# Optimization experiments

Hardware: AMD Instinct MI355X
Metric: run time of the kernel (lower is better)

## Reference

```python
import jax, jax.numpy as jnp
import numpy as np

DEPTH = 4  # truncation depth of the tensor algebra


def _tprod(a, b):
    # tensor (outer) product of level-i and level-j terms, flattened row-major
    # a: (B, C^i), b: (B, C^j) -> (B, C^(i+j))
    return (a[:, :, None] * b[:, None, :]).reshape(a.shape[0], -1)


def _exp_levels(dx):
    # exp(dx) in the truncated tensor algebra: level k = dx^{\otimes k} / k!
    levels = [dx]
    for k in range(2, DEPTH + 1):
        levels.append(_tprod(levels[-1], dx) / k)
    return tuple(levels)


def _chen(a, b):
    # Chen's identity: (a \otimes b)_k = a_k + b_k + sum_{i=1}^{k-1} a_i \otimes b_{k-i}
    out = []
    for k in range(1, DEPTH + 1):
        t = a[k - 1] + b[k - 1]
        for i in range(1, k):
            t = t + _tprod(a[i - 1], b[k - 1 - i])
        out.append(t)
    return tuple(out)


def _log_levels(s):
    # log(1 + x) = sum_{n>=1} (-1)^{n+1}/n x^{\otimes n}, x = S - 1 (levels 1..DEPTH)
    res = list(s)
    power = [t for t in s]  # x^{\otimes 1}; entries may become None (structurally zero)
    for n in range(2, DEPTH + 1):
        new = [None] * DEPTH
        for k in range(n, DEPTH + 1):
            acc = None
            for i in range(n - 1, k):
                if power[i - 1] is None:
                    continue
                term = _tprod(power[i - 1], s[k - i - 1])
                acc = term if acc is None else acc + term
            new[k - 1] = acc
        power = new
        coef = ((-1.0) ** (n + 1)) / n
        for k in range(n, DEPTH + 1):
            if power[k - 1] is not None:
                res[k - 1] = res[k - 1] + coef * power[k - 1]
    return tuple(res)


def _logsignature(path):
    # path: (B, L, C); no basepoint, stream=False, inverse=False, mode='expand'
    dxs = jnp.moveaxis(path[:, 1:] - path[:, :-1], 1, 0)  # (L-1, B, C)
    init = _exp_levels(dxs[0])

    def step(carry, dx):
        return _chen(carry, _exp_levels(dx)), None

    sig, _ = jax.lax.scan(step, init, dxs[1:])
    logsig = _log_levels(sig)
    return jnp.concatenate(logsig, axis=-1)  # (B, C + C^2 + ... + C^DEPTH)


def setup_inputs() -> dict:
    key = jax.random.key(0)
    # scale so high tensor-algebra levels stay well-conditioned in fp32
    path = 0.1 * jax.random.normal(key, (64, 256, 16), dtype=jnp.float32)
    return {"path": path}


def reference(path):
    return _logsignature(path)
```

## Files before the change

### kernel.cpp

```cpp
#include <hip/hip_runtime.h>


#define NC 16
#define NL 256
#define NB 64
#define NSTEP 255
#define OUTB 69904
#define SIG123 4368
#define OFF_L2 16
#define OFF_L3 272
#define OFF_L4 4368

#define DX1_OFF 0
#define DXT_OFF 261120
#define SIG_OFF (261120 + 262144)

__global__ __launch_bounds__(256) void k_dx(const float* __restrict__ path,
                                            float* __restrict__ dx1,
                                            float* __restrict__ dxt) {
    const int j = blockIdx.x;
    const int tid = threadIdx.x;
    __shared__ float L[NL * NC];

    const float* pj = path + (size_t)j * NL * NC;
#pragma unroll
    for (int k = 0; k < 4; ++k) {
        const int f = tid + k * 256;
        *(float4*)&L[f * 4] = *(const float4*)&pj[f * 4];
    }
    __syncthreads();

    float* d1 = dx1 + (size_t)j * NSTEP * NC;
    for (int f = tid; f < NSTEP * NC; f += 256) d1[f] = L[f + NC] - L[f];

    float* dt = dxt + (size_t)j * NC * 256;
#pragma unroll
    for (int k = 0; k < NC; ++k) {
        const int t = tid;
        if (t < NSTEP) dt[k * 256 + t] = L[(t + 1) * NC + k] - L[t * NC + k];
    }
}

__global__ __launch_bounds__(256, 4) void k_scan(const float* __restrict__ dx1,
                                                 const float* __restrict__ dxt,
                                                 float* __restrict__ out,
                                                 float* __restrict__ sig123) {
    const int bid = blockIdx.x;
    const int j = bid >> 4;
    const int a = bid & 15;
    const int tid = threadIdx.x;
    const int b = tid >> 4;
    const int c = tid & 15;

    float s4[16];
#pragma unroll
    for (int d = 0; d < 16; ++d) s4[d] = 0.f;
    float s3 = 0.f, s2ab = 0.f, s1a = 0.f;

    const float* row0 = dx1 + (size_t)j * NSTEP * NC;
    const float* ra = dxt + ((size_t)j * NC + a) * 256;
    const float* rb = dxt + ((size_t)j * NC + b) * 256;
    const float* rc = dxt + ((size_t)j * NC + c) * 256;

    int t = 0;
    for (int it = 0; it < 63; ++it, t += 4) {
        const float4 vb = *(const float4*)(rb + t);
        const float4 vc = *(const float4*)(rc + t);
        const float4 va = *(const float4*)(ra + t);
#pragma unroll
        for (int u = 0; u < 4; ++u) {
            const float* r = row0 + (t + u) * NC;
            const float4 q0 = *(const float4*)(r);
            const float4 q1 = *(const float4*)(r + 4);
            const float4 q2 = *(const float4*)(r + 8);
            const float4 q3 = *(const float4*)(r + 12);
            const float dxa = (u == 0) ? va.x : (u == 1) ? va.y : (u == 2) ? va.z : va.w;
            const float dxb = (u == 0) ? vb.x : (u == 1) ? vb.y : (u == 2) ? vb.z : vb.w;
            const float dxc = (u == 0) ? vc.x : (u == 1) ? vc.y : (u == 2) ? vc.z : vc.w;

            const float pre4 = fmaf(dxb, fmaf(1.f / 6.f, s1a, (1.f / 24.f) * dxa), 0.5f * s2ab);
            const float T = fmaf(dxc, pre4, s3);
            const float dv[16] = {q0.x, q0.y, q0.z, q0.w, q1.x, q1.y, q1.z, q1.w,
                                  q2.x, q2.y, q2.z, q2.w, q3.x, q3.y, q3.z, q3.w};
#pragma unroll
            for (int d = 0; d < 16; ++d) s4[d] = fmaf(dv[d], T, s4[d]);

            const float U = fmaf(dxb, fmaf(0.5f, s1a, (1.f / 6.f) * dxa), s2ab);
            s3 = fmaf(dxc, U, s3);
            s2ab = fmaf(dxb, fmaf(0.5f, dxa, s1a), s2ab);
            s1a += dxa;
        }
    }
    for (; t < NSTEP; ++t) {
        const float* r = row0 + t * NC;
        const float4 q0 = *(const float4*)(r);
        const float4 q1 = *(const float4*)(r + 4);
        const float4 q2 = *(const float4*)(r + 8);
        const float4 q3 = *(const float4*)(r + 12);
        const float dxa = ra[t];
        const float dxb = rb[t];
        const float dxc = rc[t];
        const float pre4 = fmaf(dxb, fmaf(1.f / 6.f, s1a, (1.f / 24.f) * dxa), 0.5f * s2ab);
        const float T = fmaf(dxc, pre4, s3);
        const float dv[16] = {q0.x, q0.y, q0.z, q0.w, q1.x, q1.y, q1.z, q1.w,
                              q2.x, q2.y, q2.z, q2.w, q3.x, q3.y, q3.z, q3.w};
#pragma unroll
        for (int d = 0; d < 16; ++d) s4[d] = fmaf(dv[d], T, s4[d]);
        const float U = fmaf(dxb, fmaf(0.5f, s1a, (1.f / 6.f) * dxa), s2ab);
        s3 = fmaf(dxc, U, s3);
        s2ab = fmaf(dxb, fmaf(0.5f, dxa, s1a), s2ab);
        s1a += dxa;
    }

    __shared__ float ls[4096];
#pragma unroll
    for (int d = 0; d < 16; d += 4)
        *(float4*)&ls[tid * 16 + d] = make_float4(s4[d], s4[d + 1], s4[d + 2], s4[d + 3]);
    __syncthreads();

    float* o4 = out + (size_t)j * OUTB + OFF_L4 + a * 4096;
#pragma unroll
    for (int k = 0; k < 4; ++k) {
        const int f = tid + k * 256;
        *(float4*)(o4 + f * 4) = *(const float4*)&ls[f * 4];
    }

    float* sg = sig123 + (size_t)j * SIG123;
    sg[OFF_L3 + (a * 16 + b) * 16 + c] = s3;
    if (c == 0) sg[OFF_L2 + a * 16 + b] = s2ab;
    if (tid == 0) sg[a] = s1a;
}

__global__ __launch_bounds__(256) void k_log(const float* __restrict__ sig123,
                                             float* __restrict__ out) {
    const int bid = blockIdx.x;
    const int j = bid >> 4;
    const int a = bid & 15;
    const int tid = threadIdx.x;

    const float* sg = sig123 + (size_t)j * SIG123;
    const float* s1 = sg;
    const float* s2 = sg + OFF_L2;
    const float* s3 = sg + OFF_L3;

    const float s1a = s1[a];
    float* outj = out + (size_t)j * OUTB;
    float* o4 = outj + OFF_L4 + a * 4096;
    const float A = -0.5f * s1a;

#pragma unroll
    for (int k = 0; k < 4; ++k) {
        const int f = tid + k * 256;
        const int m0 = f * 4;
        const int b = m0 >> 8;
        const int c = (m0 >> 4) & 15;
        const float s1b = s1[b], s1c = s1[c];
        const float s2ab = s2[a * 16 + b];
        const float s2bc = s2[b * 16 + c];
        const float s3abc = s3[m0 >> 4];
        const float s3abc_real = s3[(a * 16 + b) * 16 + c];
        (void)s3abc;

        const float Bv = fmaf((1.f / 3.f) * s1a, s1b, -0.5f * s2ab);
        const float Cv = -0.5f * s3abc_real + (1.f / 3.f) * fmaf(s1a, s2bc, s2ab * s1c)
                         - 0.25f * s1a * s1b * s1c;

        const float4 v4 = *(const float4*)(o4 + m0);
        const float4 v3 = *(const float4*)(s3 + m0);
        const float4 v2 = *(const float4*)(s2 + (m0 & 255));
        const float4 v1 = *(const float4*)(s1 + (m0 & 15));
        float4 rr;
        rr.x = fmaf(A, v3.x, v4.x) + fmaf(Bv, v2.x, Cv * v1.x);
        rr.y = fmaf(A, v3.y, v4.y) + fmaf(Bv, v2.y, Cv * v1.y);
        rr.z = fmaf(A, v3.z, v4.z) + fmaf(Bv, v2.z, Cv * v1.z);
        rr.w = fmaf(A, v3.w, v4.w) + fmaf(Bv, v2.w, Cv * v1.w);
        *(float4*)(o4 + m0) = rr;
    }

    {
        const int b = tid >> 4, c = tid & 15;
        const float s1b = s1[b], s1c = s1[c];
        const float s2ab = s2[a * 16 + b];
        const float s2bc = s2[b * 16 + c];
        const float s3abc = s3[(a * 16 + b) * 16 + c];
        const float r3 = s3abc - 0.5f * fmaf(s1a, s2bc, s2ab * s1c)
                         + (1.f / 3.f) * s1a * s1b * s1c;
        outj[OFF_L3 + a * 256 + tid] = r3;
    }
    if (tid < 16) outj[OFF_L2 + a * 16 + tid] = fmaf(-0.5f * s1a, s1[tid], s2[a * 16 + tid]);
    if (tid == 0) outj[a] = s1a;
}

extern "C" void kernel_launch(void* const* d_in, const int* in_sizes, int n_in,
                              void* d_out, int out_size, void* d_ws, size_t ws_size,
                              hipStream_t stream) {
    const float* path = (const float*)d_in[0];
    float* out = (float*)d_out;
    float* ws = (float*)d_ws;
    float* dx1 = ws + DX1_OFF;
    float* dxt = ws + DXT_OFF;
    float* sig123 = ws + SIG_OFF;

    k_dx<<<NB, 256, 0, stream>>>(path, dx1, dxt);
    k_scan<<<NB * 16, 256, 0, stream>>>(dx1, dxt, out, sig123);
    k_log<<<NB * 16, 256, 0, stream>>>(sig123, out);
}
```

Before: 124.9 us.

## Split signature scan over time halves and merge with Chen's identity

```diff
diff --git a/kernel.cpp b/kernel.cpp
--- a/kernel.cpp
+++ b/kernel.cpp
@@ -13,7 +13,10 @@
 
 #define DX1_OFF 0
 #define DXT_OFF 261120
-#define SIG_OFF (261120 + 262144)
+#define SIGA_OFF (261120 + 262144)
+#define SIGB_OFF (SIGA_OFF + NB * SIG123)
+#define B4_OFF (SIGB_OFF + NB * SIG123)
+#define WS_NEED_F ((size_t)B4_OFF + (size_t)NB * 16 * 4096)
 
 __global__ __launch_bounds__(256) void k_dx(const float* __restrict__ path,
                                             float* __restrict__ dx1,
@@ -41,17 +44,25 @@
     }
 }
 
-__global__ __launch_bounds__(256, 4) void k_scan(const float* __restrict__ dx1,
+__global__ __launch_bounds__(256, 8) void k_scan(const float* __restrict__ dx1,
                                                  const float* __restrict__ dxt,
                                                  float* __restrict__ out,
-                                                 float* __restrict__ sig123) {
-    const int bid = blockIdx.x;
+                                                 float* __restrict__ b4,
+                                                 float* __restrict__ sigA,
+                                                 float* __restrict__ sigB,
+                                                 const int split) {
+    int bid = blockIdx.x;
+    int h = 0;
+    if (split) { h = bid & 1; bid >>= 1; }
     const int j = bid >> 4;
     const int a = bid & 15;
     const int tid = threadIdx.x;
     const int b = tid >> 4;
     const int c = tid & 15;
 
+    const int t0 = h ? 128 : 0;
+    const int t1 = (split && !h) ? 128 : NSTEP;
+
     float s4[16];
 #pragma unroll
     for (int d = 0; d < 16; ++d) s4[d] = 0.f;
@@ -62,8 +73,9 @@
     const float* rb = dxt + ((size_t)j * NC + b) * 256;
     const float* rc = dxt + ((size_t)j * NC + c) * 256;
 
-    int t = 0;
-    for (int it = 0; it < 63; ++it, t += 4) {
+    int t = t0;
+    const int nv = (t1 - t0) >> 2;
+    for (int it = 0; it < nv; ++it, t += 4) {
         const float4 vb = *(const float4*)(rb + t);
         const float4 vc = *(const float4*)(rc + t);
         const float4 va = *(const float4*)(ra + t);
@@ -91,7 +103,7 @@
             s1a += dxa;
         }
     }
-    for (; t < NSTEP; ++t) {
+    for (; t < t1; ++t) {
         const float* r = row0 + t * NC;
         const float4 q0 = *(const float4*)(r);
         const float4 q1 = *(const float4*)(r + 4);
@@ -118,76 +130,116 @@
         *(float4*)&ls[tid * 16 + d] = make_float4(s4[d], s4[d + 1], s4[d + 2], s4[d + 3]);
     __syncthreads();
 
-    float* o4 = out + (size_t)j * OUTB + OFF_L4 + a * 4096;
+    float* o4 = h ? (b4 + (((size_t)j * 16 + a) << 12))
+                  : (out + (size_t)j * OUTB + OFF_L4 + a * 4096);
 #pragma unroll
     for (int k = 0; k < 4; ++k) {
         const int f = tid + k * 256;
         *(float4*)(o4 + f * 4) = *(const float4*)&ls[f * 4];
     }
 
-    float* sg = sig123 + (size_t)j * SIG123;
+    float* sg = (h ? sigB : sigA) + (size_t)j * SIG123;
     sg[OFF_L3 + (a * 16 + b) * 16 + c] = s3;
     if (c == 0) sg[OFF_L2 + a * 16 + b] = s2ab;
     if (tid == 0) sg[a] = s1a;
 }
 
-__global__ __launch_bounds__(256) void k_log(const float* __restrict__ sig123,
-                                             float* __restrict__ out) {
+__global__ __launch_bounds__(256) void k_log(const float* __restrict__ sigA,
+                                             const float* __restrict__ sigB,
+                                             const float* __restrict__ b4,
+                                             float* __restrict__ out,
+                                             const float mscale) {
     const int bid = blockIdx.x;
     const int j = bid >> 4;
     const int a = bid & 15;
     const int tid = threadIdx.x;
-
-    const float* sg = sig123 + (size_t)j * SIG123;
-    const float* s1 = sg;
-    const float* s2 = sg + OFF_L2;
-    const float* s3 = sg + OFF_L3;
-
-    const float s1a = s1[a];
+    const int q = tid >> 4;
+    const int r = tid & 15;
+
+    const float* A = sigA + (size_t)j * SIG123;
+    const float* Bp = sigB + (size_t)j * SIG123;
+
+    __shared__ float S1m[16], B1s[16], A2s[16];
+    __shared__ float S2m[256], B2s[256], A3s[256];
+    __shared__ float S3m[4096], B3s[4096];
+
+    const float b1r = mscale * Bp[r];
+    const float b2t = mscale * Bp[OFF_L2 + tid];
+
+    if (tid < 16) {
+        const float bb = mscale * Bp[tid];
+        B1s[tid] = bb;
+        S1m[tid] = A[tid] + bb;
+        A2s[tid] = A[OFF_L2 + a * 16 + tid];
+    }
+    B2s[tid] = b2t;
+    S2m[tid] = A[OFF_L2 + tid] + b2t + A[q] * b1r;
+    A3s[tid] = A[OFF_L3 + a * 256 + tid];
+#pragma unroll
+    for (int k = 0; k < 16; ++k) {
+        const int m = k * 256 + tid;
+        const float b3 = mscale * Bp[OFF_L3 + m];
+        B3s[m] = b3;
+        S3m[m] = A[OFF_L3 + m] + b3 + A[k] * b2t + A[OFF_L2 + k * 16 + q] * b1r;
+    }
+    __syncthreads();
+
+    const float s1a = S1m[a];
+    const float A1a = A[a];
+    const bool mg = (mscale != 0.f);
     float* outj = out + (size_t)j * OUTB;
     float* o4 = outj + OFF_L4 + a * 4096;
-    const float A = -0.5f * s1a;
+    const float* B4 = b4 + (((size_t)j * 16 + a) << 12);
+    const float Ac = -0.5f * s1a;
 
 #pragma unroll
     for (int k = 0; k < 4; ++k) {
         const int f = tid + k * 256;
         const int m0 = f * 4;
-        const int b = m0 >> 8;
-        const int c = (m0 >> 4) & 15;
-        const float s1b = s1[b], s1c = s1[c];
-        const float s2ab = s2[a * 16 + b];
-        const float s2bc = s2[b * 16 + c];
-        const float s3abc = s3[m0 >> 4];
-        const float s3abc_real = s3[(a * 16 + b) * 16 + c];
-        (void)s3abc;
+        const int bb = m0 >> 8;
+        const int cc = (m0 >> 4) & 15;
+        const float s1b = S1m[bb], s1c = S1m[cc];
+        const float s2ab = S2m[a * 16 + bb];
+        const float s2bc = S2m[bb * 16 + cc];
+        const float s3abc = S3m[a * 256 + (m0 >> 4)];
+        const float a3x = A3s[m0 >> 4];
+        const float a2x = A2s[bb];
+
+        const float4 a4 = *(const float4*)(o4 + m0);
+        float4 b4v = make_float4(0.f, 0.f, 0.f, 0.f);
+        if (mg) b4v = *(const float4*)(B4 + m0);
+        const float4 b3v = *(const float4*)(&B3s[m0]);
+        const float4 b2v = *(const float4*)(&B2s[m0 & 255]);
+        const float4 b1v = *(const float4*)(&B1s[m0 & 15]);
+        const float4 v3 = *(const float4*)(&S3m[m0]);
+        const float4 v2 = *(const float4*)(&S2m[m0 & 255]);
+        const float4 v1 = *(const float4*)(&S1m[m0 & 15]);
 
         const float Bv = fmaf((1.f / 3.f) * s1a, s1b, -0.5f * s2ab);
-        const float Cv = -0.5f * s3abc_real + (1.f / 3.f) * fmaf(s1a, s2bc, s2ab * s1c)
+        const float Cv = -0.5f * s3abc + (1.f / 3.f) * fmaf(s1a, s2bc, s2ab * s1c)
                          - 0.25f * s1a * s1b * s1c;
-
-        const float4 v4 = *(const float4*)(o4 + m0);
-        const float4 v3 = *(const float4*)(s3 + m0);
-        const float4 v2 = *(const float4*)(s2 + (m0 & 255));
-        const float4 v1 = *(const float4*)(s1 + (m0 & 15));
         float4 rr;
-        rr.x = fmaf(A, v3.x, v4.x) + fmaf(Bv, v2.x, Cv * v1.x);
-        rr.y = fmaf(A, v3.y, v4.y) + fmaf(Bv, v2.y, Cv * v1.y);
-        rr.z = fmaf(A, v3.z, v4.z) + fmaf(Bv, v2.z, Cv * v1.z);
-        rr.w = fmaf(A, v3.w, v4.w) + fmaf(Bv, v2.w, Cv * v1.w);
+        rr.x = a4.x + b4v.x + fmaf(A1a, b3v.x, fmaf(a2x, b2v.x, a3x * b1v.x));
+        rr.y = a4.y + b4v.y + fmaf(A1a, b3v.y, fmaf(a2x, b2v.y, a3x * b1v.y));
+        rr.z = a4.z + b4v.z + fmaf(A1a, b3v.z, fmaf(a2x, b2v.z, a3x * b1v.z));
+        rr.w = a4.w + b4v.w + fmaf(A1a, b3v.w, fmaf(a2x, b2v.w, a3x * b1v.w));
+        rr.x = fmaf(Ac, v3.x, rr.x) + fmaf(Bv, v2.x, Cv * v1.x);
+        rr.y = fmaf(Ac, v3.y, rr.y) + fmaf(Bv, v2.y, Cv * v1.y);
+        rr.z = fmaf(Ac, v3.z, rr.z) + fmaf(Bv, v2.z, Cv * v1.z);
+        rr.w = fmaf(Ac, v3.w, rr.w) + fmaf(Bv, v2.w, Cv * v1.w);
         *(float4*)(o4 + m0) = rr;
     }
 
     {
-        const int b = tid >> 4, c = tid & 15;
-        const float s1b = s1[b], s1c = s1[c];
-        const float s2ab = s2[a * 16 + b];
-        const float s2bc = s2[b * 16 + c];
-        const float s3abc = s3[(a * 16 + b) * 16 + c];
+        const float s1b = S1m[q], s1c = S1m[r];
+        const float s2ab = S2m[a * 16 + q];
+        const float s2bc = S2m[q * 16 + r];
+        const float s3abc = S3m[a * 256 + tid];
         const float r3 = s3abc - 0.5f * fmaf(s1a, s2bc, s2ab * s1c)
                          + (1.f / 3.f) * s1a * s1b * s1c;
         outj[OFF_L3 + a * 256 + tid] = r3;
     }
-    if (tid < 16) outj[OFF_L2 + a * 16 + tid] = fmaf(-0.5f * s1a, s1[tid], s2[a * 16 + tid]);
+    if (tid < 16) outj[OFF_L2 + a * 16 + tid] = fmaf(-0.5f * s1a, S1m[tid], S2m[a * 16 + tid]);
     if (tid == 0) outj[a] = s1a;
 }
 
@@ -199,9 +251,13 @@
     float* ws = (float*)d_ws;
     float* dx1 = ws + DX1_OFF;
     float* dxt = ws + DXT_OFF;
-    float* sig123 = ws + SIG_OFF;
+    float* sigA = ws + SIGA_OFF;
+
+    const int split = (ws_size >= WS_NEED_F * sizeof(float)) ? 1 : 0;
+    float* sigB = split ? (ws + SIGB_OFF) : sigA;
+    float* b4 = split ? (ws + B4_OFF) : out;
 
     k_dx<<<NB, 256, 0, stream>>>(path, dx1, dxt);
-    k_scan<<<NB * 16, 256, 0, stream>>>(dx1, dxt, out, sig123);
-    k_log<<<NB * 16, 256, 0, stream>>>(sig123, out);
-}
+    k_scan<<<split ? NB * 32 : NB * 16, 256, 0, stream>>>(dx1, dxt, out, b4, sigA, sigB, split);
+    k_log<<<NB * 16, 256, 0, stream>>>(sigA, sigB, b4, out, split ? 1.f : 0.f);
+}
```

After: 135.7 us. 8.7% more time.

## Split signature scan into four time chunks combined via Chen's identity

Applied to the files above, without the earlier changes.

```diff
diff --git a/kernel.cpp b/kernel.cpp
--- a/kernel.cpp
+++ b/kernel.cpp
@@ -4,7 +4,6 @@
 #define NC 16
 #define NL 256
 #define NB 64
-#define NSTEP 255
 #define OUTB 69904
 #define SIG123 4368
 #define OFF_L2 16
@@ -12,8 +11,10 @@
 #define OFF_L4 4368
 
 #define DX1_OFF 0
-#define DXT_OFF 261120
-#define SIG_OFF (261120 + 262144)
+#define DXT_OFF 262144
+#define SIG_OFF 524288
+
+typedef float v2f __attribute__((ext_vector_type(2)));
 
 __global__ __launch_bounds__(256) void k_dx(const float* __restrict__ path,
                                             float* __restrict__ dx1,
@@ -30,43 +31,50 @@
     }
     __syncthreads();
 
-    float* d1 = dx1 + (size_t)j * NSTEP * NC;
-    for (int f = tid; f < NSTEP * NC; f += 256) d1[f] = L[f + NC] - L[f];
+    float* d1 = dx1 + (size_t)j * NL * NC;
+#pragma unroll
+    for (int k = 0; k < 16; ++k) {
+        const int f = tid + k * 256;
+        d1[f] = (f < (NL - 1) * NC) ? (L[f + NC] - L[f]) : 0.f;
+    }
 
     float* dt = dxt + (size_t)j * NC * 256;
 #pragma unroll
     for (int k = 0; k < NC; ++k) {
         const int t = tid;
-        if (t < NSTEP) dt[k * 256 + t] = L[(t + 1) * NC + k] - L[t * NC + k];
-    }
-}
-
-__global__ __launch_bounds__(256, 4) void k_scan(const float* __restrict__ dx1,
+        dt[k * 256 + t] = (t < NL - 1) ? (L[(t + 1) * NC + k] - L[t * NC + k]) : 0.f;
+    }
+}
+
+__global__ __launch_bounds__(512, 8) void k_scan(const float* __restrict__ dx1,
                                                  const float* __restrict__ dxt,
                                                  float* __restrict__ out,
-                                                 float* __restrict__ sig123) {
+                                                 float* __restrict__ sig) {
     const int bid = blockIdx.x;
     const int j = bid >> 4;
     const int a = bid & 15;
     const int tid = threadIdx.x;
-    const int b = tid >> 4;
-    const int c = tid & 15;
-
-    float s4[16];
-#pragma unroll
-    for (int d = 0; d < 16; ++d) s4[d] = 0.f;
-    float s3 = 0.f, s2ab = 0.f, s1a = 0.f;
-
-    const float* row0 = dx1 + (size_t)j * NSTEP * NC;
+    const int qc = tid >> 7;
+    const int b = (tid >> 3) & 15;
+    const int c0 = tid & 7;
+
+    const float* row0 = dx1 + (size_t)j * NL * NC;
     const float* ra = dxt + ((size_t)j * NC + a) * 256;
     const float* rb = dxt + ((size_t)j * NC + b) * 256;
-    const float* rc = dxt + ((size_t)j * NC + c) * 256;
-
-    int t = 0;
-    for (int it = 0; it < 63; ++it, t += 4) {
+    const float* rc0 = dxt + ((size_t)j * NC + c0) * 256;
+    const float* rc1 = rc0 + 8 * 256;
+
+    v2f s4a[8], s4b[8];
+#pragma unroll
+    for (int d = 0; d < 8; ++d) { s4a[d] = (v2f){0.f, 0.f}; s4b[d] = (v2f){0.f, 0.f}; }
+    float s3_0 = 0.f, s3_1 = 0.f, s2ab = 0.f, s1a = 0.f;
+
+    int t = qc * 64;
+    for (int it = 0; it < 16; ++it, t += 4) {
+        const float4 va = *(const float4*)(ra + t);
         const float4 vb = *(const float4*)(rb + t);
-        const float4 vc = *(const float4*)(rc + t);
-        const float4 va = *(const float4*)(ra + t);
+        const float4 vc0 = *(const float4*)(rc0 + t);
+        const float4 vc1 = *(const float4*)(rc1 + t);
 #pragma unroll
         for (int u = 0; u < 4; ++u) {
             const float* r = row0 + (t + u) * NC;
@@ -76,118 +84,185 @@
             const float4 q3 = *(const float4*)(r + 12);
             const float dxa = (u == 0) ? va.x : (u == 1) ? va.y : (u == 2) ? va.z : va.w;
             const float dxb = (u == 0) ? vb.x : (u == 1) ? vb.y : (u == 2) ? vb.z : vb.w;
-            const float dxc = (u == 0) ? vc.x : (u == 1) ? vc.y : (u == 2) ? vc.z : vc.w;
-
-            const float pre4 = fmaf(dxb, fmaf(1.f / 6.f, s1a, (1.f / 24.f) * dxa), 0.5f * s2ab);
-            const float T = fmaf(dxc, pre4, s3);
-            const float dv[16] = {q0.x, q0.y, q0.z, q0.w, q1.x, q1.y, q1.z, q1.w,
-                                  q2.x, q2.y, q2.z, q2.w, q3.x, q3.y, q3.z, q3.w};
-#pragma unroll
-            for (int d = 0; d < 16; ++d) s4[d] = fmaf(dv[d], T, s4[d]);
-
-            const float U = fmaf(dxb, fmaf(0.5f, s1a, (1.f / 6.f) * dxa), s2ab);
-            s3 = fmaf(dxc, U, s3);
+            const float dxc0 = (u == 0) ? vc0.x : (u == 1) ? vc0.y : (u == 2) ? vc0.z : vc0.w;
+            const float dxc1 = (u == 0) ? vc1.x : (u == 1) ? vc1.y : (u == 2) ? vc1.z : vc1.w;
+
+            const float P = dxb * s1a;
+            const float Q = dxb * dxa;
+            const float pre4 = fmaf(1.f / 6.f, P, fmaf(1.f / 24.f, Q, 0.5f * s2ab));
+            const float U = fmaf(0.5f, P, fmaf(1.f / 6.f, Q, s2ab));
+            const float T0 = fmaf(dxc0, pre4, s3_0);
+            const float T1 = fmaf(dxc1, pre4, s3_1);
+
+            const v2f dv2[8] = {{q0.x, q0.y}, {q0.z, q0.w}, {q1.x, q1.y}, {q1.z, q1.w},
+                                {q2.x, q2.y}, {q2.z, q2.w}, {q3.x, q3.y}, {q3.z, q3.w}};
+            const v2f T0v = {T0, T0};
+            const v2f T1v = {T1, T1};
+#pragma unroll
+            for (int d = 0; d < 8; ++d) {
+                s4a[d] = __builtin_elementwise_fma(dv2[d], T0v, s4a[d]);
+                s4b[d] = __builtin_elementwise_fma(dv2[d], T1v, s4b[d]);
+            }
+            s3_0 = fmaf(dxc0, U, s3_0);
+            s3_1 = fmaf(dxc1, U, s3_1);
             s2ab = fmaf(dxb, fmaf(0.5f, dxa, s1a), s2ab);
             s1a += dxa;
         }
     }
-    for (; t < NSTEP; ++t) {
-        const float* r = row0 + t * NC;
-        const float4 q0 = *(const float4*)(r);
-        const float4 q1 = *(const float4*)(r + 4);
-        const float4 q2 = *(const float4*)(r + 8);
-        const float4 q3 = *(const float4*)(r + 12);
-        const float dxa = ra[t];
-        const float dxb = rb[t];
-        const float dxc = rc[t];
-        const float pre4 = fmaf(dxb, fmaf(1.f / 6.f, s1a, (1.f / 24.f) * dxa), 0.5f * s2ab);
-        const float T = fmaf(dxc, pre4, s3);
-        const float dv[16] = {q0.x, q0.y, q0.z, q0.w, q1.x, q1.y, q1.z, q1.w,
-                              q2.x, q2.y, q2.z, q2.w, q3.x, q3.y, q3.z, q3.w};
-#pragma unroll
-        for (int d = 0; d < 16; ++d) s4[d] = fmaf(dv[d], T, s4[d]);
-        const float U = fmaf(dxb, fmaf(0.5f, s1a, (1.f / 6.f) * dxa), s2ab);
-        s3 = fmaf(dxc, U, s3);
-        s2ab = fmaf(dxb, fmaf(0.5f, dxa, s1a), s2ab);
-        s1a += dxa;
-    }
 
     __shared__ float ls[4096];
-#pragma unroll
-    for (int d = 0; d < 16; d += 4)
-        *(float4*)&ls[tid * 16 + d] = make_float4(s4[d], s4[d + 1], s4[d + 2], s4[d + 3]);
-    __syncthreads();
-
-    float* o4 = out + (size_t)j * OUTB + OFF_L4 + a * 4096;
-#pragma unroll
-    for (int k = 0; k < 4; ++k) {
-        const int f = tid + k * 256;
-        *(float4*)(o4 + f * 4) = *(const float4*)&ls[f * 4];
-    }
-
-    float* sg = sig123 + (size_t)j * SIG123;
-    sg[OFF_L3 + (a * 16 + b) * 16 + c] = s3;
-    if (c == 0) sg[OFF_L2 + a * 16 + b] = s2ab;
-    if (tid == 0) sg[a] = s1a;
-}
-
-__global__ __launch_bounds__(256) void k_log(const float* __restrict__ sig123,
-                                             float* __restrict__ out) {
+    const int base = b * 256 + c0 * 16;
+#pragma unroll
+    for (int ph = 0; ph < 4; ++ph) {
+        if (qc == ph) {
+            if (ph == 0) {
+#pragma unroll
+                for (int d = 0; d < 4; ++d) {
+                    *(float4*)&ls[base + d * 4] = make_float4(
+                        s4a[2 * d].x, s4a[2 * d].y, s4a[2 * d + 1].x, s4a[2 * d + 1].y);
+                    *(float4*)&ls[base + 128 + d * 4] = make_float4(
+                        s4b[2 * d].x, s4b[2 * d].y, s4b[2 * d + 1].x, s4b[2 * d + 1].y);
+                }
+            } else {
+#pragma unroll
+                for (int d = 0; d < 4; ++d) {
+                    float4 v0 = *(const float4*)&ls[base + d * 4];
+                    v0.x += s4a[2 * d].x; v0.y += s4a[2 * d].y;
+                    v0.z += s4a[2 * d + 1].x; v0.w += s4a[2 * d + 1].y;
+                    *(float4*)&ls[base + d * 4] = v0;
+                    float4 v1 = *(const float4*)&ls[base + 128 + d * 4];
+                    v1.x += s4b[2 * d].x; v1.y += s4b[2 * d].y;
+                    v1.z += s4b[2 * d + 1].x; v1.w += s4b[2 * d + 1].y;
+                    *(float4*)&ls[base + 128 + d * 4] = v1;
+                }
+            }
+        }
+        __syncthreads();
+    }
+    {
+        float* o4 = out + (size_t)j * OUTB + OFF_L4 + a * 4096;
+#pragma unroll
+        for (int k = 0; k < 2; ++k) {
+            const int f = tid + k * 512;
+            *(float4*)(o4 + f * 4) = *(const float4*)&ls[f * 4];
+        }
+    }
+
+    float* sg = sig + ((size_t)qc * NB + j) * SIG123;
+    sg[OFF_L3 + (a * 16 + b) * 16 + c0] = s3_0;
+    sg[OFF_L3 + (a * 16 + b) * 16 + c0 + 8] = s3_1;
+    if (c0 == 0) sg[OFF_L2 + a * 16 + b] = s2ab;
+    if ((tid & 127) == 0) sg[a] = s1a;
+}
+
+__global__ __launch_bounds__(256, 4) void k_log(const float* __restrict__ sig,
+                                                float* __restrict__ out) {
     const int bid = blockIdx.x;
     const int j = bid >> 4;
     const int a = bid & 15;
     const int tid = threadIdx.x;
-
-    const float* sg = sig123 + (size_t)j * SIG123;
-    const float* s1 = sg;
-    const float* s2 = sg + OFF_L2;
-    const float* s3 = sg + OFF_L3;
-
-    const float s1a = s1[a];
+    const int p16 = tid >> 4;
+    const int r16 = tid & 15;
+
+    __shared__ float M1[16];
+    __shared__ float M2[256];
+    __shared__ float M3[4096];
+
+    const float* X0 = sig + (size_t)j * SIG123;
+    if (tid < 16) M1[tid] = X0[tid];
+    M2[tid] = X0[OFF_L2 + tid];
+#pragma unroll
+    for (int k = 0; k < 16; ++k) M3[k * 256 + tid] = X0[OFF_L3 + k * 256 + tid];
+
+    float4 acc[4];
+#pragma unroll
+    for (int k = 0; k < 4; ++k) acc[k] = make_float4(0.f, 0.f, 0.f, 0.f);
+    __syncthreads();
+
+    for (int s = 1; s < 4; ++s) {
+        const float* Xs = sig + ((size_t)s * NB + j) * SIG123;
+        const float m1a = M1[a];
+        float4 m3n[4];
+#pragma unroll
+        for (int k = 0; k < 4; ++k) {
+            const int f = tid + k * 256;
+            const int m0 = f * 4;
+            const int bb = m0 >> 8;
+            const int cc = (m0 >> 4) & 15;
+            const float4 x3 = *(const float4*)(Xs + OFF_L3 + m0);
+            const float4 x2 = *(const float4*)(Xs + OFF_L2 + (m0 & 255));
+            const float4 x1 = *(const float4*)(Xs + (m0 & 15));
+            const float4 m3f = *(const float4*)(&M3[m0]);
+            const float m2ab = M2[a * 16 + bb];
+            const float m3abc = M3[a * 256 + (m0 >> 4)];
+            const float m2pq = M2[bb * 16 + cc];
+            const float m1p = M1[bb];
+            acc[k].x += fmaf(m1a, x3.x, fmaf(m2ab, x2.x, m3abc * x1.x));
+            acc[k].y += fmaf(m1a, x3.y, fmaf(m2ab, x2.y, m3abc * x1.y));
+            acc[k].z += fmaf(m1a, x3.z, fmaf(m2ab, x2.z, m3abc * x1.z));
+            acc[k].w += fmaf(m1a, x3.w, fmaf(m2ab, x2.w, m3abc * x1.w));
+            m3n[k].x = m3f.x + x3.x + fmaf(m1p, x2.x, m2pq * x1.x);
+            m3n[k].y = m3f.y + x3.y + fmaf(m1p, x2.y, m2pq * x1.y);
+            m3n[k].z = m3f.z + x3.z + fmaf(m1p, x2.z, m2pq * x1.z);
+            m3n[k].w = m3f.w + x3.w + fmaf(m1p, x2.w, m2pq * x1.w);
+        }
+        const float m2new = M2[tid] + Xs[OFF_L2 + tid] + M1[p16] * Xs[r16];
+        float m1new = 0.f;
+        if (tid < 16) m1new = M1[tid] + Xs[tid];
+        __syncthreads();
+#pragma unroll
+        for (int k = 0; k < 4; ++k) *(float4*)(&M3[(tid + k * 256) * 4]) = m3n[k];
+        M2[tid] = m2new;
+        if (tid < 16) M1[tid] = m1new;
+        __syncthreads();
+    }
+
+    const float s1a = M1[a];
     float* outj = out + (size_t)j * OUTB;
     float* o4 = outj + OFF_L4 + a * 4096;
-    const float A = -0.5f * s1a;
+    const float Ac = -0.5f * s1a;
 
 #pragma unroll
     for (int k = 0; k < 4; ++k) {
         const int f = tid + k * 256;
         const int m0 = f * 4;
-        const int b = m0 >> 8;
-        const int c = (m0 >> 4) & 15;
-        const float s1b = s1[b], s1c = s1[c];
-        const float s2ab = s2[a * 16 + b];
-        const float s2bc = s2[b * 16 + c];
-        const float s3abc = s3[m0 >> 4];
-        const float s3abc_real = s3[(a * 16 + b) * 16 + c];
-        (void)s3abc;
+        const int bb = m0 >> 8;
+        const int cc = (m0 >> 4) & 15;
+        const float s1b = M1[bb], s1c = M1[cc];
+        const float s2ab = M2[a * 16 + bb];
+        const float s2bc = M2[bb * 16 + cc];
+        const float s3abc = M3[a * 256 + (m0 >> 4)];
+
+        const float4 p4 = *(const float4*)(o4 + m0);
+        const float4 v3 = *(const float4*)(&M3[m0]);
+        const float4 v2 = *(const float4*)(&M2[m0 & 255]);
+        const float4 v1 = *(const float4*)(&M1[m0 & 15]);
 
         const float Bv = fmaf((1.f / 3.f) * s1a, s1b, -0.5f * s2ab);
-        const float Cv = -0.5f * s3abc_real + (1.f / 3.f) * fmaf(s1a, s2bc, s2ab * s1c)
+        const float Cv = -0.5f * s3abc + (1.f / 3.f) * fmaf(s1a, s2bc, s2ab * s1c)
                          - 0.25f * s1a * s1b * s1c;
-
-        const float4 v4 = *(const float4*)(o4 + m0);
-        const float4 v3 = *(const float4*)(s3 + m0);
-        const float4 v2 = *(const float4*)(s2 + (m0 & 255));
-        const float4 v1 = *(const float4*)(s1 + (m0 & 15));
         float4 rr;
-        rr.x = fmaf(A, v3.x, v4.x) + fmaf(Bv, v2.x, Cv * v1.x);
-        rr.y = fmaf(A, v3.y, v4.y) + fmaf(Bv, v2.y, Cv * v1.y);
-        rr.z = fmaf(A, v3.z, v4.z) + fmaf(Bv, v2.z, Cv * v1.z);
-        rr.w = fmaf(A, v3.w, v4.w) + fmaf(Bv, v2.w, Cv * v1.w);
+        rr.x = p4.x + acc[k].x;
+        rr.y = p4.y + acc[k].y;
+        rr.z = p4.z + acc[k].z;
+        rr.w = p4.w + acc[k].w;
+        rr.x = fmaf(Ac, v3.x, rr.x) + fmaf(Bv, v2.x, Cv * v1.x);
+        rr.y = fmaf(Ac, v3.y, rr.y) + fmaf(Bv, v2.y, Cv * v1.y);
+        rr.z = fmaf(Ac, v3.z, rr.z) + fmaf(Bv, v2.z, Cv * v1.z);
+        rr.w = fmaf(Ac, v3.w, rr.w) + fmaf(Bv, v2.w, Cv * v1.w);
         *(float4*)(o4 + m0) = rr;
     }
 
     {
-        const int b = tid >> 4, c = tid & 15;
-        const float s1b = s1[b], s1c = s1[c];
-        const float s2ab = s2[a * 16 + b];
-        const float s2bc = s2[b * 16 + c];
-        const float s3abc = s3[(a * 16 + b) * 16 + c];
+        const float s1b = M1[p16], s1c = M1[r16];
+        const float s2ab = M2[a * 16 + p16];
+        const float s2bc = M2[tid];
+        const float s3abc = M3[a * 256 + tid];
         const float r3 = s3abc - 0.5f * fmaf(s1a, s2bc, s2ab * s1c)
                          + (1.f / 3.f) * s1a * s1b * s1c;
         outj[OFF_L3 + a * 256 + tid] = r3;
     }
-    if (tid < 16) outj[OFF_L2 + a * 16 + tid] = fmaf(-0.5f * s1a, s1[tid], s2[a * 16 + tid]);
+    if (tid < 16) outj[OFF_L2 + a * 16 + tid] = fmaf(-0.5f * s1a, M1[tid], M2[a * 16 + tid]);
     if (tid == 0) outj[a] = s1a;
 }
 
@@ -199,9 +274,9 @@
     float* ws = (float*)d_ws;
     float* dx1 = ws + DX1_OFF;
     float* dxt = ws + DXT_OFF;
-    float* sig123 = ws + SIG_OFF;
+    float* sig = ws + SIG_OFF;
 
     k_dx<<<NB, 256, 0, stream>>>(path, dx1, dxt);
-    k_scan<<<NB * 16, 256, 0, stream>>>(dx1, dxt, out, sig123);
-    k_log<<<NB * 16, 256, 0, stream>>>(sig123, out);
-}
+    k_scan<<<NB * 16, 512, 0, stream>>>(dx1, dxt, out, sig);
+    k_log<<<NB * 16, 256, 0, stream>>>(sig, out);
+}
```

Result: slower. 386.2 us (+209.1%).
